# Kernel optimization log

Hardware: AMD Instinct MI355X
Metric: run time of the kernel (lower is better)

The kernel has to match this reference:

```python
import jax, jax.numpy as jnp
import numpy as np

IN_C, OUT_C, N = 512, 256, 8192
NEG_INF = -1000000000.0  # matches torch's -1e9 fill


def setup_inputs() -> dict:
    key = jax.random.key(0)
    ks = jax.random.split(key, 8)
    x = jax.random.normal(ks[0], (N, IN_C), dtype=jnp.float32)
    adj = jax.random.randint(ks[1], (N, N), 0, 2, dtype=jnp.int32)
    # fc: Linear(in_c, out_c)
    lim_fc = 1.0 / np.sqrt(IN_C)
    W_fc = jax.random.uniform(ks[2], (IN_C, OUT_C), minval=-lim_fc, maxval=lim_fc, dtype=jnp.float32)
    b_fc = jax.random.uniform(ks[3], (OUT_C,), minval=-lim_fc, maxval=lim_fc, dtype=jnp.float32)
    # a1, a2: Linear(out_c, 1)
    lim_a = 1.0 / np.sqrt(OUT_C)
    W_a1 = jax.random.uniform(ks[4], (OUT_C, 1), minval=-lim_a, maxval=lim_a, dtype=jnp.float32)
    b_a1 = jax.random.uniform(ks[5], (1,), minval=-lim_a, maxval=lim_a, dtype=jnp.float32)
    W_a2 = jax.random.uniform(ks[6], (OUT_C, 1), minval=-lim_a, maxval=lim_a, dtype=jnp.float32)
    b_a2 = jax.random.uniform(ks[7], (1,), minval=-lim_a, maxval=lim_a, dtype=jnp.float32)
    return {"x": x, "adj": adj, "W_fc": W_fc, "b_fc": b_fc,
            "W_a1": W_a1, "b_a1": b_a1, "W_a2": W_a2, "b_a2": b_a2}


def reference(x, adj, W_fc, b_fc, W_a1, b_a1, W_a2, b_a2):
    h = x @ W_fc + b_fc                      # [N, out_c]
    s1 = h @ W_a1 + b_a1                     # [N, 1]
    s2 = h @ W_a2 + b_a2                     # [N, 1]
    e = jax.nn.leaky_relu(s1 + s2.T)         # [N, N], slope 0.01 matches torch default
    att = jnp.where(adj > 0, e, NEG_INF)
    att = jax.nn.softmax(att, axis=1)        # dropout omitted (eval mode)
    return att @ h                           # [N, out_c]
```

## Files before the change

### kernel.cpp

```cpp
#include <hip/hip_runtime.h>
#include <hip/hip_bf16.h>

#define IN_C 512
#define OUT_C 256
#define NN 8192
#define JSPL 8
#define JRANGE (NN / JSPL)
#define NT (JRANGE / 32)
#define L2E 1.44269504088896f

typedef __attribute__((ext_vector_type(8))) short s16x8;
typedef __attribute__((ext_vector_type(4))) float f32x4;

__device__ __forceinline__ ushort f2bf(float f) {
    unsigned u = __float_as_uint(f);
    unsigned r = (u + 0x7FFF + ((u >> 16) & 1)) >> 16;
    return (ushort)r;
}

__global__ __launch_bounds__(256) void fc_kernel(
    const float* __restrict__ x, const float* __restrict__ Wfc,
    const float* __restrict__ bfc, const float* __restrict__ Wa1,
    const float* __restrict__ ba1, const float* __restrict__ Wa2,
    const float* __restrict__ ba2,
    uint4* __restrict__ hb,
    float* __restrict__ s1, float* __restrict__ s2)
{
    __shared__ float xl[8 * IN_C];
    __shared__ float red[2][8][4];
    const int t = threadIdx.x;
    const int r0 = blockIdx.x * 8;

    {
        const float4* src = (const float4*)(x + (size_t)r0 * IN_C);
        float4* dst = (float4*)xl;
        #pragma unroll
        for (int i = 0; i < 4; i++) dst[i * 256 + t] = src[i * 256 + t];
    }
    __syncthreads();

    float acc[8];
    #pragma unroll
    for (int r = 0; r < 8; r++) acc[r] = 0.f;

    for (int c4 = 0; c4 < IN_C / 4; c4++) {
        const float w0 = Wfc[(c4 * 4 + 0) * OUT_C + t];
        const float w1 = Wfc[(c4 * 4 + 1) * OUT_C + t];
        const float w2 = Wfc[(c4 * 4 + 2) * OUT_C + t];
        const float w3 = Wfc[(c4 * 4 + 3) * OUT_C + t];
        #pragma unroll
        for (int r = 0; r < 8; r++) {
            const float4 xv = *(const float4*)&xl[r * IN_C + c4 * 4];
            acc[r] = fmaf(xv.x, w0, acc[r]);
            acc[r] = fmaf(xv.y, w1, acc[r]);
            acc[r] = fmaf(xv.z, w2, acc[r]);
            acc[r] = fmaf(xv.w, w3, acc[r]);
        }
    }
    const float bb = bfc[t];
    #pragma unroll
    for (int r = 0; r < 8; r++) acc[r] += bb;

    {
        union { ushort u[8]; uint4 v; } pk;
        #pragma unroll
        for (int r = 0; r < 8; r++) pk.u[r] = f2bf(acc[r]);
        const int jt = r0 >> 5, u = (r0 >> 3) & 3;
        hb[(size_t)jt * 1024 + u * 256 + t] = pk.v;
    }

    float p1[8], p2[8];
    const float wa1 = Wa1[t], wa2 = Wa2[t];
    #pragma unroll
    for (int r = 0; r < 8; r++) { p1[r] = acc[r] * wa1; p2[r] = acc[r] * wa2; }
    #pragma unroll
    for (int off = 32; off > 0; off >>= 1) {
        #pragma unroll
        for (int r = 0; r < 8; r++) {
            p1[r] += __shfl_down(p1[r], off);
            p2[r] += __shfl_down(p2[r], off);
        }
    }
    const int wv = t >> 6, ln = t & 63;
    if (ln == 0) {
        #pragma unroll
        for (int r = 0; r < 8; r++) { red[0][r][wv] = p1[r]; red[1][r][wv] = p2[r]; }
    }
    __syncthreads();
    if (t < 16) {
        const int s = t >> 3, r = t & 7;
        float v = red[s][r][0] + red[s][r][1] + red[s][r][2] + red[s][r][3];
        v += s ? ba2[0] : ba1[0];
        if (s) s2[r0 + r] = v; else s1[r0 + r] = v;
    }
}

__global__ __launch_bounds__(256) void smax_kernel(const float* __restrict__ s2,
                                                   float* __restrict__ smax)
{
    __shared__ float red[4];
    float m = -1e30f;
    for (int i = threadIdx.x; i < NN; i += 256) m = fmaxf(m, s2[i]);
    #pragma unroll
    for (int off = 32; off > 0; off >>= 1) m = fmaxf(m, __shfl_down(m, off));
    if ((threadIdx.x & 63) == 0) red[threadIdx.x >> 6] = m;
    __syncthreads();
    if (threadIdx.x == 0)
        smax[0] = fmaxf(fmaxf(red[0], red[1]), fmaxf(red[2], red[3]));
}

__global__ __launch_bounds__(256, 4) void attn_kernel(
    const int* __restrict__ adj, const uint4* __restrict__ hb,
    const float* __restrict__ s1, const float* __restrict__ s2,
    const float* __restrict__ smaxp, float* __restrict__ outp,
    float* __restrict__ pbase, float* __restrict__ rs)
{
    __shared__ float s2l[JRANGE];
    __shared__ unsigned long long mask_lds[64][16];

    const int t = threadIdx.x;
    const int wave = t >> 6, lane = t & 63;
    const int g = lane >> 4, lr = lane & 15;
    const int jq = blockIdx.y;
    const int Jbase = jq * JRANGE;
    const int R0 = blockIdx.x * 64;
    const int row = R0 + wave * 16 + lr;

    {
        const float4* src = (const float4*)(s2 + Jbase);
        float4* dst = (float4*)s2l;
        const float4 v = src[t];
        dst[t] = make_float4(v.x * L2E, v.y * L2E, v.z * L2E, v.w * L2E);
    }

    {
        const int wrow0 = wave * 16;
        for (int r = 0; r < 16; ++r) {
            const int* arow = adj + (size_t)(R0 + wrow0 + r) * NN + Jbase + lane;
            int v[16];
            #pragma unroll
            for (int c = 0; c < 16; ++c)
                v[c] = __builtin_nontemporal_load(arow + c * 64);
            unsigned long long myw = 0;
            #pragma unroll
            for (int c = 0; c < 16; ++c) {
                const unsigned long long m = __ballot(v[c] > 0);
                if (lane == c) myw = m;
            }
            if (lane < 16) mask_lds[wrow0 + r][lane] = myw;
        }
    }

    const float my_s1 = s1[row] * L2E;
    const float z0 = my_s1 + smaxp[0] * L2E;
    const float m_i = fmaxf(z0, 0.01f * z0);

    f32x4 acc[16];
    #pragma unroll
    for (int n = 0; n < 16; n++) acc[n] = (f32x4)(0.f);
    float rsum = 0.f;

    const uint4* hb_base = hb + (size_t)(Jbase >> 5) * 1024;

    __syncthreads();

    for (int tt = 0; tt < NT; ++tt) {
        const unsigned long long m64 = mask_lds[wave * 16 + lr][tt >> 1];
        const unsigned mb = (unsigned)(m64 >> ((tt & 1) * 32 + g * 8)) & 0xFFu;

        const int j0 = tt * 32 + g * 8;
        const float4 sva = *(const float4*)(s2l + j0);
        const float4 svb = *(const float4*)(s2l + j0 + 4);
        const float sv[8] = {sva.x, sva.y, sva.z, sva.w, svb.x, svb.y, svb.z, svb.w};
        union { ushort u[8]; s16x8 v; } pk;
        #pragma unroll
        for (int e = 0; e < 8; e++) {
            const float zz = my_s1 + sv[e];
            const float ee = fmaxf(zz, 0.01f * zz);
            float p = exp2f(ee - m_i);
            p = ((mb >> e) & 1u) ? p : 0.f;
            rsum += p;
            pk.u[e] = f2bf(p);
        }
        const s16x8 afrag = pk.v;

        const uint4* bsrc = hb_base + (size_t)tt * 1024 + g * 256 + lr;
        uint4 bf[8];
        #pragma unroll
        for (int n = 0; n < 8; n++) bf[n] = bsrc[n * 16];
        #pragma unroll
        for (int n = 0; n < 8; n++)
            acc[n] = __builtin_amdgcn_mfma_f32_16x16x32_bf16(afrag, *(const s16x8*)&bf[n], acc[n], 0, 0, 0);
        #pragma unroll
        for (int n = 0; n < 8; n++) bf[n] = bsrc[128 + n * 16];
        #pragma unroll
        for (int n = 0; n < 8; n++)
            acc[n + 8] = __builtin_amdgcn_mfma_f32_16x16x32_bf16(afrag, *(const s16x8*)&bf[n], acc[n + 8], 0, 0, 0);
    }

    rsum += __shfl_xor(rsum, 16);
    rsum += __shfl_xor(rsum, 32);
    if (g == 0) rs[(size_t)jq * NN + row] = rsum;

    float* dst = (jq == 0) ? outp : (pbase + (size_t)(jq - 1) * ((size_t)NN * OUT_C));
    #pragma unroll
    for (int r = 0; r < 4; r++) {
        const int orow = R0 + wave * 16 + g * 4 + r;
        float* op = dst + (size_t)orow * OUT_C + lr;
        #pragma unroll
        for (int n = 0; n < 16; n++)
            __builtin_nontemporal_store(acc[n][r], op + n * 16);
    }
}

__global__ __launch_bounds__(256) void combine_kernel(
    float* __restrict__ out, const float* __restrict__ pbase,
    const float* __restrict__ rs)
{
    const int row = blockIdx.x, t = threadIdx.x;
    float rsum = 0.f;
    #pragma unroll
    for (int q = 0; q < JSPL; q++) rsum += rs[(size_t)q * NN + row];
    const float inv = 1.f / rsum;
    const size_t idx = (size_t)row * OUT_C + t;
    const size_t stride = (size_t)NN * OUT_C;
    float v = out[idx];
    #pragma unroll
    for (int q = 0; q < JSPL - 1; q++)
        v += __builtin_nontemporal_load(&pbase[idx + (size_t)q * stride]);
    out[idx] = v * inv;
}

extern "C" void kernel_launch(void* const* d_in, const int* in_sizes, int n_in,
                              void* d_out, int out_size, void* d_ws, size_t ws_size,
                              hipStream_t stream) {
    const float* x   = (const float*)d_in[0];
    const int*   adj = (const int*)d_in[1];
    const float* Wfc = (const float*)d_in[2];
    const float* bfc = (const float*)d_in[3];
    const float* Wa1 = (const float*)d_in[4];
    const float* ba1 = (const float*)d_in[5];
    const float* Wa2 = (const float*)d_in[6];
    const float* ba2 = (const float*)d_in[7];
    float* out = (float*)d_out;

    char* ws = (char*)d_ws;
    uint4* hb   = (uint4*)ws;
    float* s1   = (float*)(ws + (4u << 20));
    float* s2   = s1 + NN;
    float* rs   = s2 + NN;
    float* smax = rs + JSPL * NN;
    float* pbase = (float*)(ws + (5u << 20));

    fc_kernel<<<dim3(NN / 8), 256, 0, stream>>>(x, Wfc, bfc, Wa1, ba1, Wa2, ba2, hb, s1, s2);
    smax_kernel<<<dim3(1), 256, 0, stream>>>(s2, smax);
    attn_kernel<<<dim3(NN / 64, JSPL), 256, 0, stream>>>(adj, hb, s1, s2, smax, out, pbase, rs);
    combine_kernel<<<dim3(NN), 256, 0, stream>>>(out, pbase, rs);
}
```

Baseline: 208.6 us.

## Stream adjacency directly into registers with 4-deep prefetch, halve J split

Drops the LDS staging of the adjacency bitmask and scaled s2 values. Each lane now loads its own adjacency row segment and s2 values straight into registers, with a software pipeline that prefetches four tiles ahead. The J split drops from 8 to 4, so there are fewer partial outputs for the combine step, and the occupancy hint is lowered to 2 blocks per SIMD to leave room for more registers. Risks are higher register pressure, less parallelism from fewer blocks, and uncoalesced per-row adjacency loads, since each row is now read by a single lane group.

```diff
diff --git a/kernel.cpp b/kernel.cpp
--- a/kernel.cpp
+++ b/kernel.cpp
@@ -4,13 +4,14 @@
 #define IN_C 512
 #define OUT_C 256
 #define NN 8192
-#define JSPL 8
+#define JSPL 4
 #define JRANGE (NN / JSPL)
 #define NT (JRANGE / 32)
 #define L2E 1.44269504088896f
 
 typedef __attribute__((ext_vector_type(8))) short s16x8;
 typedef __attribute__((ext_vector_type(4))) float f32x4;
+typedef __attribute__((ext_vector_type(4))) int i32x4;
 
 __device__ __forceinline__ ushort f2bf(float f) {
     unsigned u = __float_as_uint(f);
@@ -109,15 +110,12 @@
         smax[0] = fmaxf(fmaxf(red[0], red[1]), fmaxf(red[2], red[3]));
 }
 
-__global__ __launch_bounds__(256, 4) void attn_kernel(
+__global__ __launch_bounds__(256, 2) void attn_kernel(
     const int* __restrict__ adj, const uint4* __restrict__ hb,
     const float* __restrict__ s1, const float* __restrict__ s2,
     const float* __restrict__ smaxp, float* __restrict__ outp,
     float* __restrict__ pbase, float* __restrict__ rs)
 {
-    __shared__ float s2l[JRANGE];
-    __shared__ unsigned long long mask_lds[64][16];
-
     const int t = threadIdx.x;
     const int wave = t >> 6, lane = t & 63;
     const int g = lane >> 4, lr = lane & 15;
@@ -126,77 +124,73 @@
     const int R0 = blockIdx.x * 64;
     const int row = R0 + wave * 16 + lr;
 
-    {
-        const float4* src = (const float4*)(s2 + Jbase);
-        float4* dst = (float4*)s2l;
-        const float4 v = src[t];
-        dst[t] = make_float4(v.x * L2E, v.y * L2E, v.z * L2E, v.w * L2E);
-    }
-
-    {
-        const int wrow0 = wave * 16;
-        for (int r = 0; r < 16; ++r) {
-            const int* arow = adj + (size_t)(R0 + wrow0 + r) * NN + Jbase + lane;
-            int v[16];
-            #pragma unroll
-            for (int c = 0; c < 16; ++c)
-                v[c] = __builtin_nontemporal_load(arow + c * 64);
-            unsigned long long myw = 0;
-            #pragma unroll
-            for (int c = 0; c < 16; ++c) {
-                const unsigned long long m = __ballot(v[c] > 0);
-                if (lane == c) myw = m;
-            }
-            if (lane < 16) mask_lds[wrow0 + r][lane] = myw;
-        }
-    }
-
     const float my_s1 = s1[row] * L2E;
     const float z0 = my_s1 + smaxp[0] * L2E;
     const float m_i = fmaxf(z0, 0.01f * z0);
 
+    const i32x4*  arow = (const i32x4*)(adj + (size_t)row * NN + Jbase) + g * 2;
+    const float4* srow = (const float4*)(s2 + Jbase) + g * 2;
+    const uint4*  hbb  = hb + (size_t)(Jbase >> 5) * 1024 + g * 256 + lr;
+
     f32x4 acc[16];
     #pragma unroll
     for (int n = 0; n < 16; n++) acc[n] = (f32x4)(0.f);
     float rsum = 0.f;
 
-    const uint4* hb_base = hb + (size_t)(Jbase >> 5) * 1024;
-
-    __syncthreads();
-
-    for (int tt = 0; tt < NT; ++tt) {
-        const unsigned long long m64 = mask_lds[wave * 16 + lr][tt >> 1];
-        const unsigned mb = (unsigned)(m64 >> ((tt & 1) * 32 + g * 8)) & 0xFFu;
-
-        const int j0 = tt * 32 + g * 8;
-        const float4 sva = *(const float4*)(s2l + j0);
-        const float4 svb = *(const float4*)(s2l + j0 + 4);
-        const float sv[8] = {sva.x, sva.y, sva.z, sva.w, svb.x, svb.y, svb.z, svb.w};
-        union { ushort u[8]; s16x8 v; } pk;
-        #pragma unroll
-        for (int e = 0; e < 8; e++) {
-            const float zz = my_s1 + sv[e];
-            const float ee = fmaxf(zz, 0.01f * zz);
-            float p = exp2f(ee - m_i);
-            p = ((mb >> e) & 1u) ? p : 0.f;
-            rsum += p;
-            pk.u[e] = f2bf(p);
-        }
-        const s16x8 afrag = pk.v;
-
-        const uint4* bsrc = hb_base + (size_t)tt * 1024 + g * 256 + lr;
-        uint4 bf[8];
-        #pragma unroll
-        for (int n = 0; n < 8; n++) bf[n] = bsrc[n * 16];
-        #pragma unroll
-        for (int n = 0; n < 8; n++)
-            acc[n] = __builtin_amdgcn_mfma_f32_16x16x32_bf16(afrag, *(const s16x8*)&bf[n], acc[n], 0, 0, 0);
-        #pragma unroll
-        for (int n = 0; n < 8; n++) bf[n] = bsrc[128 + n * 16];
-        #pragma unroll
-        for (int n = 0; n < 8; n++)
-            acc[n + 8] = __builtin_amdgcn_mfma_f32_16x16x32_bf16(afrag, *(const s16x8*)&bf[n], acc[n + 8], 0, 0, 0);
-    }
+    i32x4 A0a = __builtin_nontemporal_load(arow + 0);
+    i32x4 A0b = __builtin_nontemporal_load(arow + 1);
+    float4 S0a = srow[0], S0b = srow[1];
+    i32x4 A1a = __builtin_nontemporal_load(arow + 8);
+    i32x4 A1b = __builtin_nontemporal_load(arow + 9);
+    float4 S1a = srow[8], S1b = srow[9];
+    i32x4 A2a = __builtin_nontemporal_load(arow + 16);
+    i32x4 A2b = __builtin_nontemporal_load(arow + 17);
+    float4 S2a = srow[16], S2b = srow[17];
+    i32x4 A3a = __builtin_nontemporal_load(arow + 24);
+    i32x4 A3b = __builtin_nontemporal_load(arow + 25);
+    float4 S3a = srow[24], S3b = srow[25];
+
+#define BODY(K, TT)                                                              \
+    {                                                                            \
+        const int av[8] = {A##K##a.x, A##K##a.y, A##K##a.z, A##K##a.w,           \
+                           A##K##b.x, A##K##b.y, A##K##b.z, A##K##b.w};          \
+        const float sv[8] = {S##K##a.x, S##K##a.y, S##K##a.z, S##K##a.w,         \
+                             S##K##b.x, S##K##b.y, S##K##b.z, S##K##b.w};        \
+        union { ushort u[8]; s16x8 v; } pk;                                      \
+        _Pragma("unroll")                                                        \
+        for (int e = 0; e < 8; e++) {                                            \
+            const float zz = fmaf(sv[e], L2E, my_s1);                            \
+            const float ee = fmaxf(zz, 0.01f * zz);                              \
+            float p = exp2f(ee - m_i);                                           \
+            p = (av[e] > 0) ? p : 0.f;                                           \
+            rsum += p;                                                           \
+            pk.u[e] = f2bf(p);                                                   \
+        }                                                                        \
+        const s16x8 afrag = pk.v;                                                \
+        const uint4* bsrc = hbb + (size_t)(TT) * 1024;                           \
+        uint4 bf[16];                                                            \
+        _Pragma("unroll")                                                        \
+        for (int n = 0; n < 16; n++) bf[n] = bsrc[n * 16];                       \
+        _Pragma("unroll")                                                        \
+        for (int n = 0; n < 16; n++)                                             \
+            acc[n] = __builtin_amdgcn_mfma_f32_16x16x32_bf16(                    \
+                afrag, *(const s16x8*)&bf[n], acc[n], 0, 0, 0);                  \
+        const int tn = ((TT) + 4 < NT) ? (TT) + 4 : 0;                           \
+        A##K##a = __builtin_nontemporal_load(arow + tn * 8);                     \
+        A##K##b = __builtin_nontemporal_load(arow + tn * 8 + 1);                 \
+        S##K##a = srow[tn * 8];                                                  \
+        S##K##b = srow[tn * 8 + 1];                                              \
+    }
+
+    #pragma unroll 1
+    for (int i = 0; i < NT / 4; ++i) {
+        const int tb = i * 4;
+        BODY(0, tb + 0)
+        BODY(1, tb + 1)
+        BODY(2, tb + 2)
+        BODY(3, tb + 3)
+    }
+#undef BODY
 
     rsum += __shfl_xor(rsum, 16);
     rsum += __shfl_xor(rsum, 32);
```

Result: slower. 225.4 us (+8.1%).
